# Optimization experiments

Measured on AMD Instinct MI355X. Metric: run time of the kernel, lower is better.

The kernel has to match this reference:

```python
import jax, jax.numpy as jnp
import numpy as np

N, E, L, H, C = 50000, 800000, 3, 4, 16
D = H * C  # 64
G = 512    # number of graphs
GRAPH_DIM = 128


def setup_inputs() -> dict:
    key = jax.random.key(0)
    ks = jax.random.split(key, 24)
    s = 0.05
    inp = {
        "x": jax.random.normal(ks[0], (N, D), jnp.float32),
        "edge_attr": jax.random.normal(ks[1], (E, 1), jnp.float32),
        "edge_index": jax.random.randint(ks[2], (2, E), 0, N, jnp.int32),
        "batch": jnp.sort(jax.random.randint(ks[3], (N,), 0, G, jnp.int32)),
        # stacked per-layer TransformerConv params (all layers have in=D)
        "Wq": s * jax.random.normal(ks[4], (L, D, D), jnp.float32),
        "bq": jnp.zeros((L, D), jnp.float32),
        "Wk": s * jax.random.normal(ks[5], (L, D, D), jnp.float32),
        "bk": jnp.zeros((L, D), jnp.float32),
        "Wv": s * jax.random.normal(ks[6], (L, D, D), jnp.float32),
        "bv": jnp.zeros((L, D), jnp.float32),
        "We": s * jax.random.normal(ks[7], (L, 1, D), jnp.float32),  # lin_edge, no bias
        "Wskip": s * jax.random.normal(ks[8], (L, D, D), jnp.float32),
        "bskip": jnp.zeros((L, D), jnp.float32),
        # graph encoder MLP head
        "W1": s * jax.random.normal(ks[9], (D, D), jnp.float32),
        "b1": jnp.zeros((D,), jnp.float32),
        "W2": s * jax.random.normal(ks[10], (D, C), jnp.float32),  # hidden_node_dim=16
        "b2": jnp.zeros((C,), jnp.float32),
        "W3": s * jax.random.normal(ks[11], (C, GRAPH_DIM), jnp.float32),
        "b3": jnp.zeros((GRAPH_DIM,), jnp.float32),
    }
    return inp


def transformer_conv(x, edge_attr, src, dst, Wq, bq, Wk, bk, Wv, bv, We, Wskip, bskip):
    # PyG TransformerConv: concat=True, beta=False, root_weight=True
    q = (x @ Wq + bq).reshape(N, H, C)
    k = (x @ Wk + bk).reshape(N, H, C)
    v = (x @ Wv + bv).reshape(N, H, C)
    e = (edge_attr @ We).reshape(E, H, C)  # lin_edge (no bias)
    kj = k[src] + e                         # [E,H,C]
    qi = q[dst]
    score = jnp.sum(qi * kj, axis=-1) / jnp.sqrt(jnp.float32(C))  # [E,H]
    # scatter softmax over edges sharing the same target node
    smax = jax.ops.segment_max(score, dst, num_segments=N)        # [N,H]
    ex = jnp.exp(score - smax[dst])
    denom = jax.ops.segment_sum(ex, dst, num_segments=N)
    alpha = ex / (denom[dst] + 1e-16)                             # [E,H]
    msg = alpha[..., None] * (v[src] + e)                         # [E,H,C]
    out = jax.ops.segment_sum(msg, dst, num_segments=N).reshape(N, D)
    return out + x @ Wskip + bskip


def reference(x, edge_attr, Wq, bq, Wk, bk, Wv, bv, We, Wskip, bskip,
              W1, b1, W2, b2, W3, b3, edge_index, batch):
    src, dst = edge_index[0], edge_index[1]
    h = x
    for l in range(L):
        h = transformer_conv(h, edge_attr, src, dst, Wq[l], bq[l], Wk[l], bk[l],
                             Wv[l], bv[l], We[l], Wskip[l], bskip[l])
        if l < L - 1:
            h = jax.nn.relu(h)
    node_embeddings = h
    # global mean pool
    sums = jax.ops.segment_sum(h, batch, num_segments=G)
    cnt = jax.ops.segment_sum(jnp.ones((N,), h.dtype), batch, num_segments=G)
    g = sums / jnp.maximum(cnt, 1.0)[:, None]
    # graph encoder MLP
    g = jax.nn.relu(g @ W1 + b1)
    g = jax.nn.relu(g @ W2 + b2)
    graph_features = g @ W3 + b3
    return node_embeddings, graph_features
```

## Files before the change

kernel.cpp:

```cpp
#include <hip/hip_runtime.h>
#include <hip/hip_fp16.h>

#define NN 50000
#define EE 800000
#define LL 3
#define HH 4
#define CC 16
#define DD 64
#define GG 512
#define GRAPH_DIM 128
#define SCAN_B 196

__global__ __launch_bounds__(256) void zero_ws(int* __restrict__ wpos,
                                               float* __restrict__ gs) {
    int i = blockIdx.x * blockDim.x + threadIdx.x;
    int stride = gridDim.x * blockDim.x;
    for (int k = i; k < NN; k += stride) wpos[k] = 0;
    for (int k = i; k < GG * 64 + GG; k += stride) gs[k] = 0.f;
}

__global__ void hist_kernel(const int* __restrict__ dst, int* __restrict__ counts) {
    int e = blockIdx.x * blockDim.x + threadIdx.x;
    if (e < EE) atomicAdd(&counts[dst[e]], 1);
}

__global__ __launch_bounds__(256) void scan_partial(const int* __restrict__ counts,
                                                    int* __restrict__ bsum) {
    __shared__ int ws[4];
    int b = blockIdx.x, t = threadIdx.x, lane = t & 63, wid = t >> 6;
    int idx = b * 256 + t;
    int x = (idx < NN) ? counts[idx] : 0;
    #pragma unroll
    for (int o = 1; o < 64; o <<= 1) x += __shfl_xor(x, o);
    if (lane == 0) ws[wid] = x;
    __syncthreads();
    if (t == 0) bsum[b] = ws[0] + ws[1] + ws[2] + ws[3];
}

__global__ __launch_bounds__(256) void scan_tops(const int* __restrict__ bsum,
                                                 int* __restrict__ boff,
                                                 int* __restrict__ row_ptr) {
    __shared__ int tmp[2][256];
    int t = threadIdx.x;
    int v = (t < SCAN_B) ? bsum[t] : 0;
    tmp[0][t] = v;
    __syncthreads();
    int src = 0;
    for (int o = 1; o < 256; o <<= 1) {
        int val = tmp[src][t];
        if (t >= o) val += tmp[src][t - o];
        tmp[src ^ 1][t] = val;
        __syncthreads();
        src ^= 1;
    }
    if (t < SCAN_B) boff[t] = tmp[src][t] - v;
    if (t == 255) row_ptr[NN] = tmp[src][255];
}

__global__ __launch_bounds__(256) void scan_final(const int* __restrict__ counts,
                                                  const int* __restrict__ boff,
                                                  int* __restrict__ row_ptr,
                                                  int* __restrict__ wpos) {
    __shared__ int ws[4];
    int b = blockIdx.x, t = threadIdx.x, lane = t & 63, wid = t >> 6;
    int idx = b * 256 + t;
    int v = (idx < NN) ? counts[idx] : 0;
    int x = v;
    #pragma unroll
    for (int o = 1; o < 64; o <<= 1) {
        int y = __shfl_up(x, o);
        if (lane >= o) x += y;
    }
    if (lane == 63) ws[wid] = x;
    __syncthreads();
    int add = boff[b];
    #pragma unroll
    for (int w = 0; w < 4; ++w) add += (w < wid) ? ws[w] : 0;
    int excl = x - v + add;
    if (idx < NN) { row_ptr[idx] = excl; wpos[idx] = excl; }
}

__global__ void scatter_kernel(const int* __restrict__ ei, const float* __restrict__ attr,
                               int* __restrict__ writepos,
                               int* __restrict__ src_s, float* __restrict__ attr_s) {
    int e = blockIdx.x * blockDim.x + threadIdx.x;
    if (e < EE) {
        int s = ei[e];
        int d = ei[EE + e];
        int p = atomicAdd(&writepos[d], 1);
        src_s[p] = s;
        attr_s[p] = attr[e];
    }
}

__global__ __launch_bounds__(256) void node_gemm(
    const float* __restrict__ hx,
    const float* __restrict__ Wq, const float* __restrict__ bq,
    const float* __restrict__ Wk, const float* __restrict__ bk,
    const float* __restrict__ Wv, const float* __restrict__ bv,
    const float* __restrict__ Ws, const float* __restrict__ bs,
    float* __restrict__ q, __half* __restrict__ kvh, float* __restrict__ sk)
{
    __shared__ float xs[32 * 64];
    int t = threadIdx.x;
    int node0 = blockIdx.x * 32;

    const float4* src4 = (const float4*)(hx + (size_t)node0 * 64);
    float4* dst4 = (float4*)xs;
    #pragma unroll
    for (int r = 0; r < 2; ++r) {
        int i4 = t + r * 256;
        int node = node0 + (i4 >> 4);
        float4 val = make_float4(0.f, 0.f, 0.f, 0.f);
        if (node < NN) val = src4[i4];
        dst4[i4] = val;
    }
    __syncthreads();

    int mat = t >> 6, j = t & 63;
    const float* W = (mat == 0) ? Wq : (mat == 1) ? Wk : (mat == 2) ? Wv : Ws;
    const float* B = (mat == 0) ? bq : (mat == 1) ? bk : (mat == 2) ? bv : bs;

    float wcol[64];
    #pragma unroll
    for (int i = 0; i < 64; ++i) wcol[i] = W[i * 64 + j];
    float bj = B[j];

    for (int n = 0; n < 32; ++n) {
        int node = node0 + n;
        if (node >= NN) break;
        float acc = bj;
        const float4* xr = (const float4*)(xs + n * 64);
        #pragma unroll
        for (int i4 = 0; i4 < 16; ++i4) {
            float4 xv = xr[i4];
            acc = fmaf(xv.x, wcol[4 * i4 + 0], acc);
            acc = fmaf(xv.y, wcol[4 * i4 + 1], acc);
            acc = fmaf(xv.z, wcol[4 * i4 + 2], acc);
            acc = fmaf(xv.w, wcol[4 * i4 + 3], acc);
        }
        size_t idx = (size_t)node * 64 + j;
        if (mat == 0)      q[idx]  = acc;
        else if (mat == 3) sk[idx] = acc;
        else kvh[idx * 2 + (mat == 2)] = __float2half_rn(acc);
    }
}

static __device__ __forceinline__ float2 h2f2(unsigned u) {
    __half2 h = __builtin_bit_cast(__half2, u);
    return __half22float2(h);
}

static __device__ __forceinline__ int cidx(int e, int p0, int p1) {
    int hi = max(p1 - 1, p0);
    int i = min(e, hi);
    return min(i, EE - 1);
}

static __device__ __forceinline__ void chunk16(
    uint4 u0, uint4 u1, uint4 u2, uint4 u3,
    float4 q0, float4 q1, float4 q2, float4 q3,
    float a, float qw, int e, int p1,
    float* accv, float& den, float& saw)
{
    float vt[16];
    float sc = 0.f;
    float2 f;
    f = h2f2(u0.x); sc = fmaf(q0.x, f.x, sc); vt[0]  = f.y;
    f = h2f2(u0.y); sc = fmaf(q0.y, f.x, sc); vt[1]  = f.y;
    f = h2f2(u0.z); sc = fmaf(q0.z, f.x, sc); vt[2]  = f.y;
    f = h2f2(u0.w); sc = fmaf(q0.w, f.x, sc); vt[3]  = f.y;
    f = h2f2(u1.x); sc = fmaf(q1.x, f.x, sc); vt[4]  = f.y;
    f = h2f2(u1.y); sc = fmaf(q1.y, f.x, sc); vt[5]  = f.y;
    f = h2f2(u1.z); sc = fmaf(q1.z, f.x, sc); vt[6]  = f.y;
    f = h2f2(u1.w); sc = fmaf(q1.w, f.x, sc); vt[7]  = f.y;
    f = h2f2(u2.x); sc = fmaf(q2.x, f.x, sc); vt[8]  = f.y;
    f = h2f2(u2.y); sc = fmaf(q2.y, f.x, sc); vt[9]  = f.y;
    f = h2f2(u2.z); sc = fmaf(q2.z, f.x, sc); vt[10] = f.y;
    f = h2f2(u2.w); sc = fmaf(q2.w, f.x, sc); vt[11] = f.y;
    f = h2f2(u3.x); sc = fmaf(q3.x, f.x, sc); vt[12] = f.y;
    f = h2f2(u3.y); sc = fmaf(q3.y, f.x, sc); vt[13] = f.y;
    f = h2f2(u3.z); sc = fmaf(q3.z, f.x, sc); vt[14] = f.y;
    f = h2f2(u3.w); sc = fmaf(q3.w, f.x, sc); vt[15] = f.y;

    float w = __expf(fmaf(a, qw, sc) * 0.25f);
    if (e >= p1) w = 0.f;
    den += w;
    saw = fmaf(w, a, saw);
    #pragma unroll
    for (int j = 0; j < 16; ++j) accv[j] = fmaf(w, vt[j], accv[j]);
}

#define ATTN_BLOCKS 1536

__global__ __launch_bounds__(256) void node_attn(
    const float* __restrict__ q, const __half* __restrict__ kvh,
    const float* __restrict__ sk, const float* __restrict__ We,
    const int* __restrict__ row_ptr, const int* __restrict__ src_s,
    const float* __restrict__ attr_s,
    float* __restrict__ out, int do_relu, int do_pool,
    const int* __restrict__ batch,
    float* __restrict__ gsum, float* __restrict__ gcnt)
{
    __shared__ float lds[4 * 16 * 68];
    int wid   = threadIdx.x >> 6;
    int lane  = threadIdx.x & 63;
    int eslot = lane & 15;
    int head  = lane >> 4;

    const int NW = ATTN_BLOCKS * 4;
    int node = blockIdx.x * 4 + wid;
    if (node >= NN) return;

    float* buf = lds + wid * (16 * 68);
    const __half* kvbase = kvh + head * 32;
    const float4* wep = (const float4*)(We + head * 16);

    int n1 = node + NW;     int n1c = (n1 < NN) ? n1 : node;
    int n2 = node + 2 * NW; int n2c = (n2 < NN) ? n2 : node;
    int p0c = row_ptr[node], p1c = row_ptr[node + 1];
    int p0n = row_ptr[n1c],  p1n = row_ptr[n1c + 1];
    int p0n2 = row_ptr[n2c], p1n2 = row_ptr[n2c + 1];

    int i0 = cidx(p0c + eslot, p0c, p1c);
    int i1 = cidx(p0c + 16 + eslot, p0c, p1c);
    int   s0c = src_s[i0]; float a0c = attr_s[i0];
    int   s1c = src_s[i1]; float a1c = attr_s[i1];
    int j0 = cidx(p0n + eslot, p0n, p1n);
    int j1 = cidx(p0n + 16 + eslot, p0n, p1n);
    int   s0n = src_s[j0]; float a0n = attr_s[j0];
    int   s1n = src_s[j1]; float a1n = attr_s[j1];

    const float4* qp = (const float4*)(q + (size_t)node * 64 + head * 16);
    float4 qc0 = qp[0], qc1 = qp[1], qc2 = qp[2], qc3 = qp[3];
    float skc = sk[(size_t)node * 64 + lane];

    const uint4* kvp0 = (const uint4*)(kvbase + (size_t)s0c * 128);
    uint4 u0 = kvp0[0], u1 = kvp0[1], u2 = kvp0[2], u3 = kvp0[3];

    for (;;) {
        int nx1 = node + NW;
        int nx3 = node + 3 * NW;
        int nx1c = (nx1 < NN) ? nx1 : node;
        int nx3c = (nx3 < NN) ? nx3 : node;

        const uint4* kvb = (const uint4*)(kvbase + (size_t)s1c * 128);
        uint4 x0 = kvb[0], x1 = kvb[1], x2 = kvb[2], x3 = kvb[3];
        const uint4* kvn = (const uint4*)(kvbase + (size_t)s0n * 128);
        uint4 un0 = kvn[0], un1 = kvn[1], un2 = kvn[2], un3 = kvn[3];
        int p0n3 = row_ptr[nx3c], p1n3 = row_ptr[nx3c + 1];
        int k0 = cidx(p0n2 + eslot, p0n2, p1n2);
        int k1 = cidx(p0n2 + 16 + eslot, p0n2, p1n2);
        int   s0n2 = src_s[k0]; float a0n2 = attr_s[k0];
        int   s1n2 = src_s[k1]; float a1n2 = attr_s[k1];
        const float4* qpn = (const float4*)(q + (size_t)nx1c * 64 + head * 16);
        float4 qn0 = qpn[0], qn1 = qpn[1], qn2 = qpn[2], qn3 = qpn[3];
        float skn = sk[(size_t)nx1c * 64 + lane];
        float4 w0 = wep[0], w1 = wep[1], w2 = wep[2], w3 = wep[3];
        float wec = We[lane];

        float qw = qc0.x * w0.x;
        qw = fmaf(qc0.y, w0.y, qw); qw = fmaf(qc0.z, w0.z, qw); qw = fmaf(qc0.w, w0.w, qw);
        qw = fmaf(qc1.x, w1.x, qw); qw = fmaf(qc1.y, w1.y, qw); qw = fmaf(qc1.z, w1.z, qw); qw = fmaf(qc1.w, w1.w, qw);
        qw = fmaf(qc2.x, w2.x, qw); qw = fmaf(qc2.y, w2.y, qw); qw = fmaf(qc2.z, w2.z, qw); qw = fmaf(qc2.w, w2.w, qw);
        qw = fmaf(qc3.x, w3.x, qw); qw = fmaf(qc3.y, w3.y, qw); qw = fmaf(qc3.z, w3.z, qw); qw = fmaf(qc3.w, w3.w, qw);

        float accv[16];
        #pragma unroll
        for (int j = 0; j < 16; ++j) accv[j] = 0.f;
        float den = 0.f, saw = 0.f;

        chunk16(u0, u1, u2, u3, qc0, qc1, qc2, qc3,
                a0c, qw, p0c + eslot, p1c, accv, den, saw);
        chunk16(x0, x1, x2, x3, qc0, qc1, qc2, qc3,
                a1c, qw, p0c + 16 + eslot, p1c, accv, den, saw);

        #pragma unroll 1
        for (int p = p0c + 32; p < p1c; p += 16) {
            int e = p + eslot;
            int i = cidx(e, p0c, p1c);
            int s = src_s[i];
            float a = attr_s[i];
            const uint4* kr = (const uint4*)(kvbase + (size_t)s * 128);
            uint4 r0 = kr[0], r1 = kr[1], r2 = kr[2], r3 = kr[3];
            chunk16(r0, r1, r2, r3, qc0, qc1, qc2, qc3,
                    a, qw, e, p1c, accv, den, saw);
        }

        den += __shfl_xor(den, 1); den += __shfl_xor(den, 2);
        den += __shfl_xor(den, 4); den += __shfl_xor(den, 8);
        saw += __shfl_xor(saw, 1); saw += __shfl_xor(saw, 2);
        saw += __shfl_xor(saw, 4); saw += __shfl_xor(saw, 8);

        float4* bw = (float4*)(buf + eslot * 68 + head * 16);
        bw[0] = make_float4(accv[0],  accv[1],  accv[2],  accv[3]);
        bw[1] = make_float4(accv[4],  accv[5],  accv[6],  accv[7]);
        bw[2] = make_float4(accv[8],  accv[9],  accv[10], accv[11]);
        bw[3] = make_float4(accv[12], accv[13], accv[14], accv[15]);
        float tot = 0.f;
        #pragma unroll
        for (int e2 = 0; e2 < 16; ++e2) tot += buf[e2 * 68 + lane];

        float o = fmaf(saw, wec, tot) / (den + 1e-16f) + skc;
        if (do_relu) o = fmaxf(o, 0.f);
        out[(size_t)node * 64 + lane] = o;

        if (do_pool) {
            int b = batch[node];
            atomicAdd(&gsum[(size_t)b * 64 + lane], o);
            if (lane == 0) atomicAdd(&gcnt[b], 1.f);
        }

        node = nx1;
        if (node >= NN) break;
        p0c = p0n;  p1c = p1n;
        p0n = p0n2; p1n = p1n2;
        p0n2 = p0n3; p1n2 = p1n3;
        s0c = s0n;  a0c = a0n;  s1c = s1n;  a1c = a1n;
        s0n = s0n2; a0n = a0n2; s1n = s1n2; a1n = a1n2;
        qc0 = qn0; qc1 = qn1; qc2 = qn2; qc3 = qn3;
        skc = skn;
        u0 = un0; u1 = un1; u2 = un2; u3 = un3;
    }
}

__global__ __launch_bounds__(128) void pool_mlp(
    const float* __restrict__ gsum, const float* __restrict__ gcnt,
    const float* __restrict__ W1, const float* __restrict__ b1,
    const float* __restrict__ W2, const float* __restrict__ b2,
    const float* __restrict__ W3, const float* __restrict__ b3,
    float* __restrict__ out)
{
    __shared__ float g[64];
    __shared__ float h1s[64];
    __shared__ float h2s[16];
    int b = blockIdx.x, t = threadIdx.x;

    if (t < 64) {
        float c = gcnt[b];
        g[t] = gsum[(size_t)b * 64 + t] / fmaxf(c, 1.f);
    }
    __syncthreads();
    if (t < 64) {
        float a = b1[t];
        #pragma unroll
        for (int i = 0; i < 64; ++i) a = fmaf(g[i], W1[i * 64 + t], a);
        h1s[t] = fmaxf(a, 0.f);
    }
    __syncthreads();
    if (t < 16) {
        float a = b2[t];
        #pragma unroll
        for (int i = 0; i < 64; ++i) a = fmaf(h1s[i], W2[i * 16 + t], a);
        h2s[t] = fmaxf(a, 0.f);
    }
    __syncthreads();
    float a = b3[t];
    #pragma unroll
    for (int i = 0; i < 16; ++i) a = fmaf(h2s[i], W3[i * 128 + t], a);
    out[(size_t)b * 128 + t] = a;
}

extern "C" void kernel_launch(void* const* d_in, const int* in_sizes, int n_in,
                              void* d_out, int out_size, void* d_ws, size_t ws_size,
                              hipStream_t stream) {
    const float* x         = (const float*)d_in[0];
    const float* edge_attr = (const float*)d_in[1];
    const int*   edge_index= (const int*)d_in[2];
    const int*   batch     = (const int*)d_in[3];
    const float* Wq   = (const float*)d_in[4];
    const float* bq   = (const float*)d_in[5];
    const float* Wk   = (const float*)d_in[6];
    const float* bk   = (const float*)d_in[7];
    const float* Wv   = (const float*)d_in[8];
    const float* bv   = (const float*)d_in[9];
    const float* We   = (const float*)d_in[10];
    const float* Wsk  = (const float*)d_in[11];
    const float* bsk  = (const float*)d_in[12];
    const float* W1   = (const float*)d_in[13];
    const float* b1   = (const float*)d_in[14];
    const float* W2   = (const float*)d_in[15];
    const float* b2   = (const float*)d_in[16];
    const float* W3   = (const float*)d_in[17];
    const float* b3   = (const float*)d_in[18];

    float* out        = (float*)d_out;
    float* node_emb   = out;
    float* graph_feat = out + (size_t)NN * 64;

    float* wsf    = (float*)d_ws;
    float* q      = wsf;
    float* kvf    = q    + (size_t)NN * 64;
    float* skp    = kvf  + (size_t)NN * 64;
    float* h      = skp  + (size_t)NN * 64;
    float* attr_s = h    + (size_t)NN * 64;
    int*   src_s  = (int*)(attr_s + EE);
    int*   row_ptr= src_s + EE;
    int*   wpos   = row_ptr + (NN + 1);
    float* gsum   = (float*)(wpos + NN);
    float* gcnt   = gsum + (size_t)GG * 64;
    int*   bsum   = (int*)(gcnt + GG);
    int*   boff   = bsum + 256;
    __half* kvh   = (__half*)kvf;

    zero_ws<<<256, 256, 0, stream>>>(wpos, gsum);
    hist_kernel<<<(EE + 255) / 256, 256, 0, stream>>>(edge_index + EE, wpos);
    scan_partial<<<SCAN_B, 256, 0, stream>>>(wpos, bsum);
    scan_tops<<<1, 256, 0, stream>>>(bsum, boff, row_ptr);
    scan_final<<<SCAN_B, 256, 0, stream>>>(wpos, boff, row_ptr, wpos);
    scatter_kernel<<<(EE + 255) / 256, 256, 0, stream>>>(edge_index, edge_attr,
                                                         wpos, src_s, attr_s);

    int gemm_grid = (NN + 31) / 32;

    const float* layer_in = x;
    for (int l = 0; l < LL; ++l) {
        const float* Wq_l = Wq + (size_t)l * 64 * 64;
        const float* Wk_l = Wk + (size_t)l * 64 * 64;
        const float* Wv_l = Wv + (size_t)l * 64 * 64;
        const float* Ws_l = Wsk + (size_t)l * 64 * 64;
        const float* bq_l = bq + (size_t)l * 64;
        const float* bk_l = bk + (size_t)l * 64;
        const float* bv_l = bv + (size_t)l * 64;
        const float* bs_l = bsk + (size_t)l * 64;
        const float* We_l = We + (size_t)l * 64;

        node_gemm<<<gemm_grid, 256, 0, stream>>>(layer_in,
            Wq_l, bq_l, Wk_l, bk_l, Wv_l, bv_l, Ws_l, bs_l,
            q, kvh, skp);

        int last = (l == LL - 1);
        float* dst_h = last ? node_emb : h;
        node_attn<<<ATTN_BLOCKS, 256, 0, stream>>>(q, kvh, skp, We_l,
            row_ptr, src_s, attr_s,
            dst_h, !last, last,
            batch, gsum, gcnt);

        layer_in = h;
    }

    pool_mlp<<<GG, 128, 0, stream>>>(gsum, gcnt, W1, b1, W2, b2, W3, b3, graph_feat);
}
```

Baseline: 492.8 us.

## Rewrite node projection GEMM with fp16 MFMA matrix-core instructions

Replaces the scalar FMA node_gemm (shared-memory staged inputs, one output column per thread) with a wave-level MFMA 16x16x32 f16 kernel. Each wave computes one of the four 64x64 projections for 64 nodes, loading activations and weights directly from global memory and converting them to fp16. This targets the FMA-bound per-layer projection cost. It lowers input precision to fp16, which may perturb accuracy, and it adds uncoalesced strided weight loads.

```diff
diff --git a/kernel.cpp b/kernel.cpp
--- a/kernel.cpp
+++ b/kernel.cpp
@@ -10,6 +10,9 @@
 #define GG 512
 #define GRAPH_DIM 128
 #define SCAN_B 196
+
+typedef __attribute__((ext_vector_type(8))) _Float16 f16x8;
+typedef __attribute__((ext_vector_type(4))) float f32x4;
 
 __global__ __launch_bounds__(256) void zero_ws(int* __restrict__ wpos,
                                                float* __restrict__ gs) {
@@ -101,48 +104,83 @@
     const float* __restrict__ Ws, const float* __restrict__ bs,
     float* __restrict__ q, __half* __restrict__ kvh, float* __restrict__ sk)
 {
-    __shared__ float xs[32 * 64];
-    int t = threadIdx.x;
-    int node0 = blockIdx.x * 32;
-
-    const float4* src4 = (const float4*)(hx + (size_t)node0 * 64);
-    float4* dst4 = (float4*)xs;
-    #pragma unroll
-    for (int r = 0; r < 2; ++r) {
-        int i4 = t + r * 256;
-        int node = node0 + (i4 >> 4);
-        float4 val = make_float4(0.f, 0.f, 0.f, 0.f);
-        if (node < NN) val = src4[i4];
-        dst4[i4] = val;
-    }
-    __syncthreads();
-
-    int mat = t >> 6, j = t & 63;
-    const float* W = (mat == 0) ? Wq : (mat == 1) ? Wk : (mat == 2) ? Wv : Ws;
-    const float* B = (mat == 0) ? bq : (mat == 1) ? bk : (mat == 2) ? bv : bs;
-
-    float wcol[64];
-    #pragma unroll
-    for (int i = 0; i < 64; ++i) wcol[i] = W[i * 64 + j];
-    float bj = B[j];
-
-    for (int n = 0; n < 32; ++n) {
-        int node = node0 + n;
-        if (node >= NN) break;
-        float acc = bj;
-        const float4* xr = (const float4*)(xs + n * 64);
-        #pragma unroll
-        for (int i4 = 0; i4 < 16; ++i4) {
-            float4 xv = xr[i4];
-            acc = fmaf(xv.x, wcol[4 * i4 + 0], acc);
-            acc = fmaf(xv.y, wcol[4 * i4 + 1], acc);
-            acc = fmaf(xv.z, wcol[4 * i4 + 2], acc);
-            acc = fmaf(xv.w, wcol[4 * i4 + 3], acc);
-        }
-        size_t idx = (size_t)node * 64 + j;
-        if (mat == 0)      q[idx]  = acc;
-        else if (mat == 3) sk[idx] = acc;
-        else kvh[idx * 2 + (mat == 2)] = __float2half_rn(acc);
+    int wave = threadIdx.x >> 6;
+    int lane = threadIdx.x & 63;
+    int l15 = lane & 15, lg = lane >> 4;
+    int node0 = blockIdx.x * 64;
+
+    const float* W  = (wave == 0) ? Wq : (wave == 1) ? Wk : (wave == 2) ? Wv : Ws;
+    const float* Bv = (wave == 0) ? bq : (wave == 1) ? bk : (wave == 2) ? bv : bs;
+
+    f16x8 af[4][2];
+    #pragma unroll
+    for (int mt = 0; mt < 4; ++mt) {
+        int row = node0 + mt * 16 + l15;
+        row = min(row, NN - 1);
+        const float4* hp = (const float4*)(hx + (size_t)row * 64);
+        #pragma unroll
+        for (int ks = 0; ks < 2; ++ks) {
+            float4 a0 = hp[ks * 8 + lg * 2];
+            float4 a1 = hp[ks * 8 + lg * 2 + 1];
+            f16x8 f;
+            f[0] = (_Float16)a0.x; f[1] = (_Float16)a0.y;
+            f[2] = (_Float16)a0.z; f[3] = (_Float16)a0.w;
+            f[4] = (_Float16)a1.x; f[5] = (_Float16)a1.y;
+            f[6] = (_Float16)a1.z; f[7] = (_Float16)a1.w;
+            af[mt][ks] = f;
+        }
+    }
+
+    f16x8 bf[4][2];
+    #pragma unroll
+    for (int nt = 0; nt < 4; ++nt) {
+        #pragma unroll
+        for (int ks = 0; ks < 2; ++ks) {
+            const float* wp = W + (size_t)(ks * 32 + lg * 8) * 64 + nt * 16 + l15;
+            f16x8 f;
+            #pragma unroll
+            for (int j = 0; j < 8; ++j) f[j] = (_Float16)wp[j * 64];
+            bf[nt][ks] = f;
+        }
+    }
+
+    f32x4 acc[4][4];
+    #pragma unroll
+    for (int nt = 0; nt < 4; ++nt) {
+        float b = Bv[nt * 16 + l15];
+        #pragma unroll
+        for (int mt = 0; mt < 4; ++mt) {
+            acc[mt][nt][0] = b; acc[mt][nt][1] = b;
+            acc[mt][nt][2] = b; acc[mt][nt][3] = b;
+        }
+    }
+
+    #pragma unroll
+    for (int mt = 0; mt < 4; ++mt)
+        #pragma unroll
+        for (int nt = 0; nt < 4; ++nt)
+            #pragma unroll
+            for (int ks = 0; ks < 2; ++ks)
+                acc[mt][nt] = __builtin_amdgcn_mfma_f32_16x16x32_f16(
+                    af[mt][ks], bf[nt][ks], acc[mt][nt], 0, 0, 0);
+
+    #pragma unroll
+    for (int mt = 0; mt < 4; ++mt) {
+        #pragma unroll
+        for (int r = 0; r < 4; ++r) {
+            int node = node0 + mt * 16 + lg * 4 + r;
+            if (node < NN) {
+                size_t nb = (size_t)node * 64;
+                #pragma unroll
+                for (int nt = 0; nt < 4; ++nt) {
+                    int col = nt * 16 + l15;
+                    float v = acc[mt][nt][r];
+                    if (wave == 0)      q[nb + col] = v;
+                    else if (wave == 3) sk[nb + col] = v;
+                    else kvh[(nb + col) * 2 + (wave == 2)] = __float2half_rn(v);
+                }
+            }
+        }
     }
 }
 
@@ -411,7 +449,7 @@
     scatter_kernel<<<(EE + 255) / 256, 256, 0, stream>>>(edge_index, edge_attr,
                                                          wpos, src_s, attr_s);
 
-    int gemm_grid = (NN + 31) / 32;
+    int gemm_grid = (NN + 63) / 64;
 
     const float* layer_in = x;
     for (int l = 0; l < LL; ++l) {
```

After: 448.1 us. -9.1%, faster.
